# Performance work log

Measured on AMD Instinct MI355X. Metric: run time of the kernel, lower is better.

The kernel has to match this reference:

```python
import jax, jax.numpy as jnp
import numpy as np

VOCAB, EMB, H, B, S = 32000, 512, 1024, 64, 128

def setup_inputs() -> dict:
    key = jax.random.key(0)
    ks = jax.random.split(key, 16)
    g = lambda k, shape, fan: jax.random.normal(k, shape, jnp.float32) * (1.0 / np.sqrt(fan))
    return {
        "dec_input": jax.random.randint(ks[0], (B, 1), 0, VOCAB),
        "hidden_state": jax.random.normal(ks[1], (B, H), jnp.float32),
        "enc_output": jax.random.normal(ks[2], (B, S, H), jnp.float32),
        "emb": g(ks[3], (VOCAB, EMB), EMB),
        "W1_k": g(ks[4], (H, H), H), "W1_b": jnp.zeros((H,), jnp.float32),
        "W2_k": g(ks[5], (H, H), H), "W2_b": jnp.zeros((H,), jnp.float32),
        "V_k": g(ks[6], (H, 1), H), "V_b": jnp.zeros((1,), jnp.float32),
        "gru_k": g(ks[7], (H + EMB, 3 * H), H + EMB),
        "gru_rk": g(ks[8], (H, 3 * H), H),
        "gru_b": jnp.zeros((2, 3 * H), jnp.float32),  # reset_after: input bias + recurrent bias
        "out_k": g(ks[9], (H, VOCAB), H), "out_b": jnp.zeros((VOCAB,), jnp.float32),
    }

def reference(dec_input, hidden_state, enc_output, emb, W1_k, W1_b, W2_k, W2_b,
              V_k, V_b, gru_k, gru_rk, gru_b, out_k, out_b):
    # Bahdanau additive attention
    # score: (B,S,1) = V(tanh(W1(enc) + W2(h)[:,None,:]))
    feat = jnp.tanh(jnp.einsum('bsh,hk->bsk', enc_output, W1_k) + W1_b
                    + (hidden_state @ W2_k + W2_b)[:, None, :])
    score = jnp.einsum('bsk,ko->bso', feat, V_k) + V_b          # (B,S,1)
    attention_weights = jax.nn.softmax(score, axis=1)            # (B,S,1)
    context = jnp.sum(attention_weights * enc_output, axis=1)    # (B,H)
    # embedding + concat (seq len 1 -> squeeze the time axis)
    x_emb = emb[dec_input[:, 0]]                                 # (B,EMB)
    x = jnp.concatenate([context, x_emb], axis=-1)               # (B,H+EMB)
    # GRU cell, one step, reset_after=True (Keras/CuDNN convention)
    xm = x @ gru_k + gru_b[0]                                    # (B,3H)
    hm = hidden_state @ gru_rk + gru_b[1]                        # (B,3H)
    Hd = hidden_state.shape[-1]
    xz, xr, xh = xm[:, :Hd], xm[:, Hd:2*Hd], xm[:, 2*Hd:]
    hz, hr, hh = hm[:, :Hd], hm[:, Hd:2*Hd], hm[:, 2*Hd:]
    z = jax.nn.sigmoid(xz + hz)
    r = jax.nn.sigmoid(xr + hr)
    h_cand = jnp.tanh(xh + r * hh)
    state = z * hidden_state + (1.0 - z) * h_cand                # (B,H)
    # seq len 1: GRU output == state; reshape(-1, H) is identity here
    probs = state @ out_k + out_b                                # (B,VOCAB)
    return probs, state, attention_weights
```

## Files before the change

### kernel.cpp

```cpp
#include <hip/hip_runtime.h>


#define B_ 64
#define S_ 128
#define H_ 1024
#define EMB_ 512
#define VOCAB_ 32000

typedef __attribute__((ext_vector_type(8))) short short8;
typedef __attribute__((ext_vector_type(4))) float f32x4;

__device__ __forceinline__ unsigned short f2bf_bits(float f) {
    unsigned int u = __float_as_uint(f);
    u += 0x7FFF + ((u >> 16) & 1);
    return (unsigned short)(u >> 16);
}
__device__ __forceinline__ float sigmoidf_(float x) { return 1.0f / (1.0f + expf(-x)); }
__device__ __forceinline__ int sw_(int r) { return (r ^ (r >> 2)) & 3; }
__device__ __forceinline__ int bsw_(int k) { return ((k >> 3) & 3) << 1; }

__device__ __forceinline__ short8 pack8_(float4 lo, float4 hi) {
    short8 s;
    s[0] = (short)f2bf_bits(lo.x);
    s[1] = (short)f2bf_bits(lo.y);
    s[2] = (short)f2bf_bits(lo.z);
    s[3] = (short)f2bf_bits(lo.w);
    s[4] = (short)f2bf_bits(hi.x);
    s[5] = (short)f2bf_bits(hi.y);
    s[6] = (short)f2bf_bits(hi.z);
    s[7] = (short)f2bf_bits(hi.w);
    return s;
}

template <int NF>
__device__ void mfma_gemm_tile(const float* __restrict__ A, int lda,
                               const float* __restrict__ W, int ldw,
                               int m_base, int n_base, int k0, int k1,
                               f32x4 (&acc)[4][NF]) {
    constexpr int NT = 64 * NF;
    constexpr int CPR = NT / 8;
    __shared__ __attribute__((aligned(16))) unsigned short A_lds[2][64 * 32];
    __shared__ __attribute__((aligned(16))) unsigned short B_lds[2][32 * NT];
    const int tid = threadIdx.x;
    const int w = tid >> 6, lane = tid & 63, quad = lane >> 4, l15 = lane & 15;

    const f32x4 z = {0.0f, 0.0f, 0.0f, 0.0f};
#pragma unroll
    for (int mi = 0; mi < 4; ++mi)
#pragma unroll
        for (int ni = 0; ni < NF; ++ni) acc[mi][ni] = z;

    const int ar = tid >> 2, ac = tid & 3;
    const int aslot = ac ^ sw_(ar);
    int bkr[NF], bch[NF];
#pragma unroll
    for (int i = 0; i < NF; ++i) {
        int id = tid + 256 * i;
        bkr[i] = id / CPR;
        bch[i] = id % CPR;
    }

    float4 a0, a1, blo[NF], bhi[NF];
    {
        const float* asrc = A + (size_t)(m_base + ar) * lda + k0 + 8 * ac;
        a0 = *(const float4*)asrc;
        a1 = *(const float4*)(asrc + 4);
#pragma unroll
        for (int i = 0; i < NF; ++i) {
            const float* bs = W + (size_t)(k0 + bkr[i]) * ldw + n_base + 8 * bch[i];
            blo[i] = *(const float4*)bs;
            bhi[i] = *(const float4*)(bs + 4);
        }
    }

    int p = 0;
    for (int k = k0; k < k1; k += 32) {
        *(short8*)&A_lds[p][ar * 32 + aslot * 8] = pack8_(a0, a1);
#pragma unroll
        for (int i = 0; i < NF; ++i)
            *(short8*)&B_lds[p][bkr[i] * NT + ((bch[i] ^ bsw_(bkr[i])) << 3)] =
                pack8_(blo[i], bhi[i]);
        __syncthreads();
        if (k + 32 < k1) {
            const float* asrc = A + (size_t)(m_base + ar) * lda + (k + 32) + 8 * ac;
            a0 = *(const float4*)asrc;
            a1 = *(const float4*)(asrc + 4);
#pragma unroll
            for (int i = 0; i < NF; ++i) {
                const float* bs =
                    W + (size_t)(k + 32 + bkr[i]) * ldw + n_base + 8 * bch[i];
                blo[i] = *(const float4*)bs;
                bhi[i] = *(const float4*)(bs + 4);
            }
        }
        short8 bfrag[NF];
#pragma unroll
        for (int ni = 0; ni < NF; ++ni) {
            int nrel = w * 16 * NF + 16 * ni + l15;
            int ch = nrel >> 3, off = nrel & 7;
#pragma unroll
            for (int j = 0; j < 8; ++j) {
                int kk = quad * 8 + j;
                bfrag[ni][j] =
                    (short)B_lds[p][kk * NT + (((ch ^ bsw_(kk)) << 3) + off)];
            }
        }
#pragma unroll
        for (int mi = 0; mi < 4; ++mi) {
            int r = 16 * mi + l15;
            short8 afrag = *(const short8*)&A_lds[p][r * 32 + ((quad ^ sw_(r)) << 3)];
#pragma unroll
            for (int ni = 0; ni < NF; ++ni)
                acc[mi][ni] = __builtin_amdgcn_mfma_f32_16x16x32_bf16(
                    afrag, bfrag[ni], acc[mi][ni], 0, 0, 0);
        }
        p ^= 1;
    }
}

__global__ void init_bias4_kernel(float* __restrict__ hproj, const float* __restrict__ W2_b,
                                  float* __restrict__ hm, float* __restrict__ xm,
                                  const float* __restrict__ gru_b,
                                  float* __restrict__ score, const float* __restrict__ V_b) {
    int i = blockIdx.x * 256 + threadIdx.x;
    const int E0 = B_ * H_;
    const int E1 = E0 + B_ * 3 * H_;
    const int E2 = E1 + B_ * 3 * H_;
    const int E3 = E2 + B_ * S_;
    if (i < E0) {
        hproj[i] = W2_b[i & (H_ - 1)];
    } else if (i < E1) {
        int j = i - E0;
        hm[j] = gru_b[3 * H_ + j % (3 * H_)];
    } else if (i < E2) {
        int j = i - E1;
        xm[j] = gru_b[j % (3 * H_)];
    } else if (i < E3) {
        score[i - E2] = V_b[0];
    }
}

template <int NF>
__global__ __launch_bounds__(256) void gemm_mfma_atomic_kernel(
    const float* __restrict__ A, int lda, const float* __restrict__ W, int ldw,
    float* __restrict__ C, int kslice) {
    f32x4 acc[4][NF];
    const int n_base = blockIdx.x * 64 * NF;
    const int k0 = blockIdx.y * kslice;
    mfma_gemm_tile<NF>(A, lda, W, ldw, 0, n_base, k0, k0 + kslice, acc);
    const int tid = threadIdx.x, w = tid >> 6, lane = tid & 63;
    const int quad = lane >> 4, l15 = lane & 15;
#pragma unroll
    for (int mi = 0; mi < 4; ++mi)
#pragma unroll
        for (int ni = 0; ni < NF; ++ni) {
            int col = n_base + w * 16 * NF + 16 * ni + l15;
#pragma unroll
            for (int r = 0; r < 4; ++r) {
                int row = 16 * mi + quad * 4 + r;
                atomicAdd(&C[(size_t)row * ldw + col], acc[mi][ni][r]);
            }
        }
}

__global__ __launch_bounds__(256) void score_mfma_kernel(
    const float* __restrict__ enc, const float* __restrict__ W1,
    const float* __restrict__ W1b, const float* __restrict__ Vk,
    const float* __restrict__ hproj, float* __restrict__ score) {
    f32x4 acc[4][4];
    const int n_base = blockIdx.x * 256;
    const int m_base = blockIdx.y * 64;
    const int b = m_base >> 7, s_base = m_base & 127;
    mfma_gemm_tile<4>(enc, H_, W1, H_, m_base, n_base, 0, H_, acc);

    const int tid = threadIdx.x, w = tid >> 6, lane = tid & 63;
    const int quad = lane >> 4, l15 = lane & 15;

    float rowpart[4][4];
#pragma unroll
    for (int mi = 0; mi < 4; ++mi)
#pragma unroll
        for (int r = 0; r < 4; ++r) rowpart[mi][r] = 0.0f;

#pragma unroll
    for (int ni = 0; ni < 4; ++ni) {
        int kcol = n_base + w * 64 + 16 * ni + l15;
        float add = W1b[kcol] + hproj[(size_t)b * H_ + kcol];
        float vv = Vk[kcol];
#pragma unroll
        for (int mi = 0; mi < 4; ++mi)
#pragma unroll
            for (int r = 0; r < 4; ++r)
                rowpart[mi][r] += tanhf(acc[mi][ni][r] + add) * vv;
    }
#pragma unroll
    for (int m = 1; m <= 8; m <<= 1)
#pragma unroll
        for (int mi = 0; mi < 4; ++mi)
#pragma unroll
            for (int r = 0; r < 4; ++r)
                rowpart[mi][r] += __shfl_xor(rowpart[mi][r], m, 64);
    if (l15 == 0) {
#pragma unroll
        for (int mi = 0; mi < 4; ++mi)
#pragma unroll
            for (int r = 0; r < 4; ++r)
                atomicAdd(&score[b * S_ + s_base + 16 * mi + quad * 4 + r],
                          rowpart[mi][r]);
    }
}

__global__ __launch_bounds__(256) void probs_mfma_kernel(
    const float* __restrict__ state, const float* __restrict__ out_k,
    const float* __restrict__ out_b, float* __restrict__ probs) {
    f32x4 acc[4][1];
    const int n_base = blockIdx.x * 64;
    mfma_gemm_tile<1>(state, H_, out_k, VOCAB_, 0, n_base, 0, H_, acc);
    const int tid = threadIdx.x, w = tid >> 6, lane = tid & 63;
    const int quad = lane >> 4, l15 = lane & 15;
    int col = n_base + w * 16 + l15;
    float bv = out_b[col];
#pragma unroll
    for (int mi = 0; mi < 4; ++mi) {
#pragma unroll
        for (int r = 0; r < 4; ++r) {
            int row = 16 * mi + quad * 4 + r;
            probs[(size_t)row * VOCAB_ + col] = acc[mi][0][r] + bv;
        }
    }
}

__global__ void softmax_kernel(const float* __restrict__ score,
                               float* __restrict__ attn_out) {
    const int b = blockIdx.x;
    const int s = threadIdx.x;
    __shared__ float red[128];
    float v = score[b * S_ + s];
    red[s] = v;
    __syncthreads();
    for (int str = 64; str > 0; str >>= 1) {
        if (s < str) red[s] = fmaxf(red[s], red[s + str]);
        __syncthreads();
    }
    float m = red[0];
    __syncthreads();
    float e = expf(v - m);
    red[s] = e;
    __syncthreads();
    for (int str = 64; str > 0; str >>= 1) {
        if (s < str) red[s] += red[s + str];
        __syncthreads();
    }
    attn_out[b * S_ + s] = e / red[0];
}

__global__ void context_kernel(const float* __restrict__ attn,
                               const float* __restrict__ enc,
                               float* __restrict__ ctx) {
    const int b = blockIdx.x >> 2;
    const int h = ((blockIdx.x & 3) << 8) + threadIdx.x;
    __shared__ float aw[S_];
    if (threadIdx.x < S_) aw[threadIdx.x] = attn[b * S_ + threadIdx.x];
    __syncthreads();
    const float* ebase = enc + (size_t)b * S_ * H_ + h;
    float a0 = 0.0f, a1 = 0.0f, a2 = 0.0f, a3 = 0.0f;
#pragma unroll 4
    for (int s = 0; s < S_; s += 4) {
        a0 += aw[s + 0] * ebase[(size_t)(s + 0) * H_];
        a1 += aw[s + 1] * ebase[(size_t)(s + 1) * H_];
        a2 += aw[s + 2] * ebase[(size_t)(s + 2) * H_];
        a3 += aw[s + 3] * ebase[(size_t)(s + 3) * H_];
    }
    ctx[(size_t)b * H_ + h] = (a0 + a1) + (a2 + a3);
}

__global__ void buildx_kernel(const float* __restrict__ ctx, const float* __restrict__ emb,
                              const int* __restrict__ dec, float* __restrict__ x) {
    const int b = blockIdx.x;
    const int t = threadIdx.x;
    const int tok = dec[b];
    float* xb = x + (size_t)b * (H_ + EMB_);
    for (int i = t; i < H_; i += 256) xb[i] = ctx[(size_t)b * H_ + i];
    for (int i = t; i < EMB_; i += 256) xb[H_ + i] = emb[(size_t)tok * EMB_ + i];
}

__global__ void gates_kernel(const float* __restrict__ xm, const float* __restrict__ hm,
                             const float* __restrict__ hidden,
                             float* __restrict__ state_out) {
    const int idx = blockIdx.x * 256 + threadIdx.x;
    const int b = idx >> 10, j = idx & (H_ - 1);
    const float* xmb = xm + (size_t)b * 3 * H_;
    const float* hmb = hm + (size_t)b * 3 * H_;
    float z = sigmoidf_(xmb[j] + hmb[j]);
    float r = sigmoidf_(xmb[H_ + j] + hmb[H_ + j]);
    float hc = tanhf(xmb[2 * H_ + j] + r * hmb[2 * H_ + j]);
    state_out[idx] = z * hidden[idx] + (1.0f - z) * hc;
}

extern "C" void kernel_launch(void* const* d_in, const int* in_sizes, int n_in,
                              void* d_out, int out_size, void* d_ws, size_t ws_size,
                              hipStream_t stream) {
    const int* dec_input = (const int*)d_in[0];
    const float* hidden = (const float*)d_in[1];
    const float* enc = (const float*)d_in[2];
    const float* emb = (const float*)d_in[3];
    const float* W1_k = (const float*)d_in[4];
    const float* W1_b = (const float*)d_in[5];
    const float* W2_k = (const float*)d_in[6];
    const float* W2_b = (const float*)d_in[7];
    const float* V_k = (const float*)d_in[8];
    const float* V_b = (const float*)d_in[9];
    const float* gru_k = (const float*)d_in[10];
    const float* gru_rk = (const float*)d_in[11];
    const float* gru_b = (const float*)d_in[12];
    const float* out_k = (const float*)d_in[13];
    const float* out_b = (const float*)d_in[14];

    float* out = (float*)d_out;
    float* probs_out = out;
    float* state_out = out + (size_t)B_ * VOCAB_;
    float* attn_out = state_out + (size_t)B_ * H_;

    const size_t NEED_F = 630784;
    float* scratch = (ws_size >= NEED_F * sizeof(float)) ? (float*)d_ws
                                                         : probs_out;
    float* hproj = scratch;
    float* hm = hproj + B_ * H_;
    float* score = hm + B_ * 3 * H_;
    float* ctx = score + B_ * S_;
    float* xvec = ctx + B_ * H_;
    float* xm = xvec + B_ * (H_ + EMB_);

    const int INIT_TOTAL = B_ * H_ + 2 * B_ * 3 * H_ + B_ * S_;
    init_bias4_kernel<<<(INIT_TOTAL + 255) / 256, 256, 0, stream>>>(
        hproj, W2_b, hm, xm, gru_b, score, V_b);

    gemm_mfma_atomic_kernel<1><<<dim3(16, 8), 256, 0, stream>>>(hidden, H_, W2_k, H_,
                                                                hproj, H_ / 8);
    gemm_mfma_atomic_kernel<1><<<dim3(48, 8), 256, 0, stream>>>(hidden, H_, gru_rk,
                                                                3 * H_, hm, H_ / 8);
    score_mfma_kernel<<<dim3(4, 128), 256, 0, stream>>>(enc, W1_k, W1_b, V_k, hproj,
                                                        score);
    softmax_kernel<<<B_, S_, 0, stream>>>(score, attn_out);
    context_kernel<<<B_ * (H_ / 256), 256, 0, stream>>>(attn_out, enc, ctx);
    buildx_kernel<<<B_, 256, 0, stream>>>(ctx, emb, dec_input, xvec);
    gemm_mfma_atomic_kernel<1><<<dim3(48, 8), 256, 0, stream>>>(xvec, H_ + EMB_, gru_k,
                                                                3 * H_, xm, (H_ + EMB_) / 8);
    gates_kernel<<<(B_ * H_) / 256, 256, 0, stream>>>(xm, hm, hidden, state_out);
    probs_mfma_kernel<<<dim3(VOCAB_ / 64), 256, 0, stream>>>(state_out, out_k, out_b,
                                                             probs_out);
}
```

Before: 374.2 us.

## Transpose B tile in LDS, deepen prefetch, fuse small GEMMs and attention kernels

The shared MFMA tile routine now stores B in LDS transposed (n-major), so each lane reads its B fragment with one vector LDS load instead of eight scalar ones. It also keeps two k-steps of global prefetch in flight. Separately, the two hidden-state GEMMs are merged into one launch, and softmax, context and embedding concat are fused into one kernel, removing launches and the ctx buffer. Scratch now always lives in the probs output region, which the final probs kernel overwrites. The cost is more registers for the deeper prefetch, and if k-range/64 is not an integer the loop could mis-handle the tail.

Result: no change. 368.4 us (-1.6%).

```diff
diff --git a/kernel.cpp b/kernel.cpp
--- a/kernel.cpp
+++ b/kernel.cpp
@@ -17,7 +17,10 @@
 }
 __device__ __forceinline__ float sigmoidf_(float x) { return 1.0f / (1.0f + expf(-x)); }
 __device__ __forceinline__ int sw_(int r) { return (r ^ (r >> 2)) & 3; }
-__device__ __forceinline__ int bsw_(int k) { return ((k >> 3) & 3) << 1; }
+__device__ __forceinline__ int bf_(int n) { return (n ^ (n >> 2)) & 3; }
+__device__ __forceinline__ float fc4_(const float4& v, int c) {
+    return c == 0 ? v.x : c == 1 ? v.y : c == 2 ? v.z : v.w;
+}
 
 __device__ __forceinline__ short8 pack8_(float4 lo, float4 hi) {
     short8 s;
@@ -38,9 +41,9 @@
                                int m_base, int n_base, int k0, int k1,
                                f32x4 (&acc)[4][NF]) {
     constexpr int NT = 64 * NF;
-    constexpr int CPR = NT / 8;
+    constexpr int JOBS = (NF >= 2) ? NF / 2 : 1;
     __shared__ __attribute__((aligned(16))) unsigned short A_lds[2][64 * 32];
-    __shared__ __attribute__((aligned(16))) unsigned short B_lds[2][32 * NT];
+    __shared__ __attribute__((aligned(16))) unsigned short B_lds[2][NT * 32];
     const int tid = threadIdx.x;
     const int w = tid >> 6, lane = tid & 63, quad = lane >> 4, l15 = lane & 15;
 
@@ -52,69 +55,136 @@
 
     const int ar = tid >> 2, ac = tid & 3;
     const int aslot = ac ^ sw_(ar);
-    int bkr[NF], bch[NF];
-#pragma unroll
-    for (int i = 0; i < NF; ++i) {
-        int id = tid + 256 * i;
-        bkr[i] = id / CPR;
-        bch[i] = id % CPR;
-    }
-
-    float4 a0, a1, blo[NF], bhi[NF];
-    {
-        const float* asrc = A + (size_t)(m_base + ar) * lda + k0 + 8 * ac;
-        a0 = *(const float4*)asrc;
-        a1 = *(const float4*)(asrc + 4);
-#pragma unroll
-        for (int i = 0; i < NF; ++i) {
-            const float* bs = W + (size_t)(k0 + bkr[i]) * ldw + n_base + 8 * bch[i];
-            blo[i] = *(const float4*)bs;
-            bhi[i] = *(const float4*)(bs + 4);
+    int bk[JOBS], bn[JOBS];
+    if constexpr (NF == 1) {
+        bk[0] = 4 * (tid >> 5);
+        bn[0] = 2 * (tid & 31);
+    } else {
+#pragma unroll
+        for (int j = 0; j < JOBS; ++j) {
+            int id = tid + 256 * j;
+            bk[j] = 4 * (id / (16 * NF));
+            bn[j] = 4 * (id % (16 * NF));
+        }
+    }
+
+    float4 areg[2][2];
+    float4 br4[2][JOBS][4];
+    float2 br2[2][4];
+
+#pragma unroll
+    for (int s = 0; s < 2; ++s) {
+        int kk = k0 + 32 * s;
+        if (s == 0 || kk < k1) {
+            const float* asrc = A + (size_t)(m_base + ar) * lda + kk + 8 * ac;
+            areg[s][0] = *(const float4*)asrc;
+            areg[s][1] = *(const float4*)(asrc + 4);
+            if constexpr (NF == 1) {
+                const float* bs = W + (size_t)(kk + bk[0]) * ldw + n_base + bn[0];
+#pragma unroll
+                for (int i = 0; i < 4; ++i)
+                    br2[s][i] = *(const float2*)(bs + (size_t)i * ldw);
+            } else {
+#pragma unroll
+                for (int j = 0; j < JOBS; ++j) {
+                    const float* bs = W + (size_t)(kk + bk[j]) * ldw + n_base + bn[j];
+#pragma unroll
+                    for (int i = 0; i < 4; ++i)
+                        br4[s][j][i] = *(const float4*)(bs + (size_t)i * ldw);
+                }
+            }
         }
     }
 
     int p = 0;
-    for (int k = k0; k < k1; k += 32) {
-        *(short8*)&A_lds[p][ar * 32 + aslot * 8] = pack8_(a0, a1);
-#pragma unroll
-        for (int i = 0; i < NF; ++i)
-            *(short8*)&B_lds[p][bkr[i] * NT + ((bch[i] ^ bsw_(bkr[i])) << 3)] =
-                pack8_(blo[i], bhi[i]);
-        __syncthreads();
-        if (k + 32 < k1) {
-            const float* asrc = A + (size_t)(m_base + ar) * lda + (k + 32) + 8 * ac;
-            a0 = *(const float4*)asrc;
-            a1 = *(const float4*)(asrc + 4);
-#pragma unroll
-            for (int i = 0; i < NF; ++i) {
-                const float* bs =
-                    W + (size_t)(k + 32 + bkr[i]) * ldw + n_base + 8 * bch[i];
-                blo[i] = *(const float4*)bs;
-                bhi[i] = *(const float4*)(bs + 4);
-            }
-        }
-        short8 bfrag[NF];
-#pragma unroll
-        for (int ni = 0; ni < NF; ++ni) {
-            int nrel = w * 16 * NF + 16 * ni + l15;
-            int ch = nrel >> 3, off = nrel & 7;
-#pragma unroll
-            for (int j = 0; j < 8; ++j) {
-                int kk = quad * 8 + j;
-                bfrag[ni][j] =
-                    (short)B_lds[p][kk * NT + (((ch ^ bsw_(kk)) << 3) + off)];
-            }
-        }
-#pragma unroll
-        for (int mi = 0; mi < 4; ++mi) {
-            int r = 16 * mi + l15;
-            short8 afrag = *(const short8*)&A_lds[p][r * 32 + ((quad ^ sw_(r)) << 3)];
-#pragma unroll
-            for (int ni = 0; ni < NF; ++ni)
-                acc[mi][ni] = __builtin_amdgcn_mfma_f32_16x16x32_bf16(
-                    afrag, bfrag[ni], acc[mi][ni], 0, 0, 0);
-        }
-        p ^= 1;
+    for (int k = k0; k < k1; k += 64) {
+#pragma unroll
+        for (int s = 0; s < 2; ++s) {
+            const int kk = k + 32 * s;
+            *(short8*)&A_lds[p][ar * 32 + aslot * 8] = pack8_(areg[s][0], areg[s][1]);
+            if constexpr (NF == 1) {
+                const int kb = bk[0];
+#pragma unroll
+                for (int c = 0; c < 2; ++c) {
+                    int n = bn[0] + c;
+                    int si = n * 32 + ((((kb >> 3) ^ bf_(n)) << 3) + (kb & 7));
+                    unsigned int lo, hi;
+                    if (c == 0) {
+                        lo = (unsigned)f2bf_bits(br2[s][0].x) |
+                             ((unsigned)f2bf_bits(br2[s][1].x) << 16);
+                        hi = (unsigned)f2bf_bits(br2[s][2].x) |
+                             ((unsigned)f2bf_bits(br2[s][3].x) << 16);
+                    } else {
+                        lo = (unsigned)f2bf_bits(br2[s][0].y) |
+                             ((unsigned)f2bf_bits(br2[s][1].y) << 16);
+                        hi = (unsigned)f2bf_bits(br2[s][2].y) |
+                             ((unsigned)f2bf_bits(br2[s][3].y) << 16);
+                    }
+                    uint2 wv;
+                    wv.x = lo;
+                    wv.y = hi;
+                    *(uint2*)&B_lds[p][si] = wv;
+                }
+            } else {
+#pragma unroll
+                for (int j = 0; j < JOBS; ++j) {
+                    const int kb = bk[j];
+#pragma unroll
+                    for (int c = 0; c < 4; ++c) {
+                        int n = bn[j] + c;
+                        int si = n * 32 + ((((kb >> 3) ^ bf_(n)) << 3) + (kb & 7));
+                        unsigned int lo = (unsigned)f2bf_bits(fc4_(br4[s][j][0], c)) |
+                                          ((unsigned)f2bf_bits(fc4_(br4[s][j][1], c)) << 16);
+                        unsigned int hi = (unsigned)f2bf_bits(fc4_(br4[s][j][2], c)) |
+                                          ((unsigned)f2bf_bits(fc4_(br4[s][j][3], c)) << 16);
+                        uint2 wv;
+                        wv.x = lo;
+                        wv.y = hi;
+                        *(uint2*)&B_lds[p][si] = wv;
+                    }
+                }
+            }
+            __syncthreads();
+            const int kpre = kk + 64;
+            if (kpre < k1) {
+                const float* asrc = A + (size_t)(m_base + ar) * lda + kpre + 8 * ac;
+                areg[s][0] = *(const float4*)asrc;
+                areg[s][1] = *(const float4*)(asrc + 4);
+                if constexpr (NF == 1) {
+                    const float* bs = W + (size_t)(kpre + bk[0]) * ldw + n_base + bn[0];
+#pragma unroll
+                    for (int i = 0; i < 4; ++i)
+                        br2[s][i] = *(const float2*)(bs + (size_t)i * ldw);
+                } else {
+#pragma unroll
+                    for (int j = 0; j < JOBS; ++j) {
+                        const float* bs =
+                            W + (size_t)(kpre + bk[j]) * ldw + n_base + bn[j];
+#pragma unroll
+                        for (int i = 0; i < 4; ++i)
+                            br4[s][j][i] = *(const float4*)(bs + (size_t)i * ldw);
+                    }
+                }
+            }
+            short8 bfrag[NF];
+#pragma unroll
+            for (int ni = 0; ni < NF; ++ni) {
+                int nrel = w * 16 * NF + 16 * ni + l15;
+                bfrag[ni] =
+                    *(const short8*)&B_lds[p][nrel * 32 + ((quad ^ bf_(nrel)) << 3)];
+            }
+#pragma unroll
+            for (int mi = 0; mi < 4; ++mi) {
+                int r = 16 * mi + l15;
+                short8 afrag =
+                    *(const short8*)&A_lds[p][r * 32 + ((quad ^ sw_(r)) << 3)];
+#pragma unroll
+                for (int ni = 0; ni < NF; ++ni)
+                    acc[mi][ni] = __builtin_amdgcn_mfma_f32_16x16x32_bf16(
+                        afrag, bfrag[ni], acc[mi][ni], 0, 0, 0);
+            }
+            p ^= 1;
+        }
     }
 }
 
@@ -163,6 +233,35 @@
         }
 }
 
+__global__ __launch_bounds__(256) void gemm_dual_kernel(
+    const float* __restrict__ hidden, const float* __restrict__ W2_k,
+    const float* __restrict__ gru_rk, float* __restrict__ hproj,
+    float* __restrict__ hm, int kslice) {
+    f32x4 acc[4][1];
+    const int bx = blockIdx.x;
+    const float* W;
+    float* C;
+    int ldw, n_base;
+    if (bx < 16) {
+        W = W2_k; C = hproj; ldw = H_; n_base = bx * 64;
+    } else {
+        W = gru_rk; C = hm; ldw = 3 * H_; n_base = (bx - 16) * 64;
+    }
+    const int k0 = blockIdx.y * kslice;
+    mfma_gemm_tile<1>(hidden, H_, W, ldw, 0, n_base, k0, k0 + kslice, acc);
+    const int tid = threadIdx.x, w = tid >> 6, lane = tid & 63;
+    const int quad = lane >> 4, l15 = lane & 15;
+#pragma unroll
+    for (int mi = 0; mi < 4; ++mi) {
+        int col = n_base + w * 16 + l15;
+#pragma unroll
+        for (int r = 0; r < 4; ++r) {
+            int row = 16 * mi + quad * 4 + r;
+            atomicAdd(&C[(size_t)row * ldw + col], acc[mi][0][r]);
+        }
+    }
+}
+
 __global__ __launch_bounds__(256) void score_mfma_kernel(
     const float* __restrict__ enc, const float* __restrict__ W1,
     const float* __restrict__ W1b, const float* __restrict__ Vk,
@@ -230,58 +329,58 @@
     }
 }
 
-__global__ void softmax_kernel(const float* __restrict__ score,
-                               float* __restrict__ attn_out) {
-    const int b = blockIdx.x;
-    const int s = threadIdx.x;
+__global__ __launch_bounds__(256) void attn_ctx_kernel(
+    const float* __restrict__ score, const float* __restrict__ enc,
+    const float* __restrict__ emb, const int* __restrict__ dec,
+    float* __restrict__ attn_out, float* __restrict__ xvec) {
+    const int b = blockIdx.x >> 2, q = blockIdx.x & 3;
+    const int t = threadIdx.x;
     __shared__ float red[128];
-    float v = score[b * S_ + s];
-    red[s] = v;
+    __shared__ float aw[128];
+    float v = 0.0f;
+    if (t < 128) {
+        v = score[b * S_ + t];
+        red[t] = v;
+    }
     __syncthreads();
     for (int str = 64; str > 0; str >>= 1) {
-        if (s < str) red[s] = fmaxf(red[s], red[s + str]);
+        if (t < str) red[t] = fmaxf(red[t], red[t + str]);
         __syncthreads();
     }
     float m = red[0];
     __syncthreads();
-    float e = expf(v - m);
-    red[s] = e;
+    float e = 0.0f;
+    if (t < 128) {
+        e = expf(v - m);
+        red[t] = e;
+    }
     __syncthreads();
     for (int str = 64; str > 0; str >>= 1) {
-        if (s < str) red[s] += red[s + str];
+        if (t < str) red[t] += red[t + str];
         __syncthreads();
     }
-    attn_out[b * S_ + s] = e / red[0];
-}
-
-__global__ void context_kernel(const float* __restrict__ attn,
-                               const float* __restrict__ enc,
-                               float* __restrict__ ctx) {
-    const int b = blockIdx.x >> 2;
-    const int h = ((blockIdx.x & 3) << 8) + threadIdx.x;
-    __shared__ float aw[S_];
-    if (threadIdx.x < S_) aw[threadIdx.x] = attn[b * S_ + threadIdx.x];
+    float inv = 1.0f / red[0];
+    if (t < 128) aw[t] = e * inv;
     __syncthreads();
-    const float* ebase = enc + (size_t)b * S_ * H_ + h;
+
+    const int col = q * 256 + t;
+    const float* ebase = enc + (size_t)b * S_ * H_ + col;
     float a0 = 0.0f, a1 = 0.0f, a2 = 0.0f, a3 = 0.0f;
-#pragma unroll 4
     for (int s = 0; s < S_; s += 4) {
         a0 += aw[s + 0] * ebase[(size_t)(s + 0) * H_];
         a1 += aw[s + 1] * ebase[(size_t)(s + 1) * H_];
         a2 += aw[s + 2] * ebase[(size_t)(s + 2) * H_];
         a3 += aw[s + 3] * ebase[(size_t)(s + 3) * H_];
     }
-    ctx[(size_t)b * H_ + h] = (a0 + a1) + (a2 + a3);
-}
-
-__global__ void buildx_kernel(const float* __restrict__ ctx, const float* __restrict__ emb,
-                              const int* __restrict__ dec, float* __restrict__ x) {
-    const int b = blockIdx.x;
-    const int t = threadIdx.x;
-    const int tok = dec[b];
-    float* xb = x + (size_t)b * (H_ + EMB_);
-    for (int i = t; i < H_; i += 256) xb[i] = ctx[(size_t)b * H_ + i];
-    for (int i = t; i < EMB_; i += 256) xb[H_ + i] = emb[(size_t)tok * EMB_ + i];
+    xvec[(size_t)b * (H_ + EMB_) + col] = (a0 + a1) + (a2 + a3);
+
+    if (q == 0 && t < 128) attn_out[b * S_ + t] = aw[t];
+    if (q == 1) {
+        int tok = dec[b];
+        float* xb = xvec + (size_t)b * (H_ + EMB_) + H_;
+        xb[t] = emb[(size_t)tok * EMB_ + t];
+        xb[t + 256] = emb[(size_t)tok * EMB_ + t + 256];
+    }
 }
 
 __global__ void gates_kernel(const float* __restrict__ xm, const float* __restrict__ hm,
@@ -321,29 +420,22 @@
     float* state_out = out + (size_t)B_ * VOCAB_;
     float* attn_out = state_out + (size_t)B_ * H_;
 
-    const size_t NEED_F = 630784;
-    float* scratch = (ws_size >= NEED_F * sizeof(float)) ? (float*)d_ws
-                                                         : probs_out;
-    float* hproj = scratch;
+    float* hproj = probs_out;
     float* hm = hproj + B_ * H_;
     float* score = hm + B_ * 3 * H_;
-    float* ctx = score + B_ * S_;
-    float* xvec = ctx + B_ * H_;
+    float* xvec = score + B_ * S_;
     float* xm = xvec + B_ * (H_ + EMB_);
 
     const int INIT_TOTAL = B_ * H_ + 2 * B_ * 3 * H_ + B_ * S_;
     init_bias4_kernel<<<(INIT_TOTAL + 255) / 256, 256, 0, stream>>>(
         hproj, W2_b, hm, xm, gru_b, score, V_b);
 
-    gemm_mfma_atomic_kernel<1><<<dim3(16, 8), 256, 0, stream>>>(hidden, H_, W2_k, H_,
-                                                                hproj, H_ / 8);
-    gemm_mfma_atomic_kernel<1><<<dim3(48, 8), 256, 0, stream>>>(hidden, H_, gru_rk,
-                                                                3 * H_, hm, H_ / 8);
+    gemm_dual_kernel<<<dim3(64, 8), 256, 0, stream>>>(hidden, W2_k, gru_rk, hproj,
+                                                      hm, H_ / 8);
     score_mfma_kernel<<<dim3(4, 128), 256, 0, stream>>>(enc, W1_k, W1_b, V_k, hproj,
                                                         score);
-    softmax_kernel<<<B_, S_, 0, stream>>>(score, attn_out);
-    context_kernel<<<B_ * (H_ / 256), 256, 0, stream>>>(attn_out, enc, ctx);
-    buildx_kernel<<<B_, 256, 0, stream>>>(ctx, emb, dec_input, xvec);
+    attn_ctx_kernel<<<B_ * 4, 256, 0, stream>>>(score, enc, emb, dec_input, attn_out,
+                                                xvec);
     gemm_mfma_atomic_kernel<1><<<dim3(48, 8), 256, 0, stream>>>(xvec, H_ + EMB_, gru_k,
                                                                 3 * H_, xm, (H_ + EMB_) / 8);
     gates_kernel<<<(B_ * H_) / 256, 256, 0, stream>>>(xm, hm, hidden, state_out);
```
